# Kernel tuning notes

Measured on AMD Instinct MI355X. Metric: run time of the kernel, lower is better.

## Reference

```python
import jax, jax.numpy as jnp
import numpy as np

NUM_CLASSES = 19  # number of distinct labels in targets (fill_max)


def setup_inputs() -> dict:
    key = jax.random.key(0)
    k1, k2 = jax.random.split(key)
    n, d = 262144, 128
    inputs = jax.random.normal(k1, (n, d), dtype=jnp.float32)
    targets = jax.random.randint(k2, (n,), 0, NUM_CLASSES, dtype=jnp.int64)
    return {"inputs": inputs, "targets": targets}


def reference(inputs, targets):
    # Same math as the O(n^2) torch loop: for each sample i, the center is the
    # mean of all samples sharing targets[i]. Computed as one segment-reduction
    # over labels followed by a gather.
    n = inputs.shape[0]
    sums = jax.ops.segment_sum(inputs, targets, num_segments=NUM_CLASSES)          # [C, d]
    counts = jax.ops.segment_sum(jnp.ones((n,), inputs.dtype), targets,
                                 num_segments=NUM_CLASSES)                          # [C]
    class_centers = sums / counts[:, None]                                          # [C, d]
    centers = class_centers[targets]                                                # [n, d]
    dist_pc = jnp.sqrt(jnp.sum((inputs - centers) ** 2, axis=1))                    # [n]
    return jnp.mean(dist_pc)
```

## Files before the change

### kernel.cpp

```cpp
#include <hip/hip_runtime.h>
#include <math.h>

#define NCLS 19
#define DIM  128
#define CD   (NCLS * DIM)
#define WPB  16

__global__ __launch_bounds__(1024) void k_accum(const float2* __restrict__ in2,
                                                const int* __restrict__ tgt,
                                                float* __restrict__ gsums,
                                                int* __restrict__ gcounts,
                                                int n) {
    __shared__ float ls[WPB * CD];
    __shared__ int   lcnt[WPB * NCLS];
    const int tid  = threadIdx.x;
    const int w    = tid >> 6;
    const int lane = tid & 63;
    float* tbl = &ls[w * CD];
    int*   cnt = &lcnt[w * NCLS];

    for (int i = tid; i < WPB * CD; i += 1024) ls[i] = 0.0f;
    for (int i = tid; i < WPB * NCLS; i += 1024) lcnt[i] = 0;
    __syncthreads();

    const int stride = gridDim.x * WPB;
    for (int row = blockIdx.x * WPB + w; row < n; row += stride) {
        float2 v = in2[(size_t)row * 64 + lane];
        int c = tgt[row];
        float2 cur = *(float2*)&tbl[c * DIM + lane * 2];
        cur.x += v.x;
        cur.y += v.y;
        *(float2*)&tbl[c * DIM + lane * 2] = cur;
        if (lane == 0) cnt[c]++;
    }
    __syncthreads();

    for (int i = tid; i < CD; i += 1024) {
        float s = 0.0f;
        #pragma unroll
        for (int ww = 0; ww < WPB; ww++) s += ls[ww * CD + i];
        unsafeAtomicAdd(&gsums[i], s);
    }
    if (tid < NCLS) {
        int s = 0;
        #pragma unroll
        for (int ww = 0; ww < WPB; ww++) s += lcnt[ww * NCLS + tid];
        atomicAdd(&gcounts[tid], s);
    }
}

__global__ __launch_bounds__(256) void k_dist(const float4* __restrict__ in4,
                                              const int* __restrict__ tgt,
                                              const float* __restrict__ gsums,
                                              const int* __restrict__ gcounts,
                                              float* __restrict__ out,
                                              int n, float inv_n) {
    __shared__ __align__(16) float lcent[CD];
    __shared__ float red[256];
    const int tid = threadIdx.x;

    for (int i = tid; i < CD; i += 256)
        lcent[i] = gsums[i] / (float)gcounts[i >> 7];
    __syncthreads();

    const int l32 = tid & 31;
    const int rib = tid >> 5;
    const int stride = gridDim.x * 8;
    float acc = 0.0f;

    for (int row = blockIdx.x * 8 + rib; row < n; row += stride) {
        float4 v = in4[(size_t)row * 32 + l32];
        int c = tgt[row];
        float4 ce = *(const float4*)&lcent[c * DIM + l32 * 4];
        float dx = v.x - ce.x, dy = v.y - ce.y, dz = v.z - ce.z, dw = v.w - ce.w;
        float d2 = dx * dx + dy * dy + dz * dz + dw * dw;
        for (int off = 16; off > 0; off >>= 1)
            d2 += __shfl_down(d2, off, 32);
        if (l32 == 0) acc += sqrtf(d2);
    }

    red[tid] = acc;
    __syncthreads();
    for (int s = 128; s > 0; s >>= 1) {
        if (tid < s) red[tid] += red[tid + s];
        __syncthreads();
    }
    if (tid == 0) unsafeAtomicAdd(out, red[0] * inv_n);
}

extern "C" void kernel_launch(void* const* d_in, const int* in_sizes, int n_in,
                              void* d_out, int out_size, void* d_ws, size_t ws_size,
                              hipStream_t stream) {
    const float* in  = (const float*)d_in[0];
    const int*   tgt = (const int*)d_in[1];
    const int n = in_sizes[0] / DIM;

    float* gsums   = (float*)d_ws;
    int*   gcounts = (int*)(gsums + CD);
    float* out     = (float*)d_out;

    hipMemsetAsync(d_ws, 0, CD * sizeof(float) + NCLS * sizeof(int), stream);
    hipMemsetAsync(d_out, 0, sizeof(float), stream);

    k_accum<<<256, 1024, 0, stream>>>((const float2*)in, tgt, gsums, gcounts, n);
    k_dist<<<1024, 256, 0, stream>>>((const float4*)in, tgt, gsums, gcounts, out,
                                     n, 1.0f / (float)n);
}
```

Before: 238.5 us.

## Restructure accumulation to 32-lane float4 groups and unroll both kernels by four rows

The accumulation kernel moves from 1024-thread blocks with 64-lane float2 private tables to 256-thread blocks with 32-lane float4 groups, each keeping its own shared-memory table, and the grid doubles to 512 blocks. Both the accumulation and distance loops are unrolled four ways so four row loads are in flight before they are used, aiming to hide global memory latency in this bandwidth-bound pass. Smaller per-block LDS use may allow more blocks per CU, but there are fewer private tables per block and more global atomics from the extra blocks.

```diff
diff --git a/kernel.cpp b/kernel.cpp
--- a/kernel.cpp
+++ b/kernel.cpp
@@ -4,47 +4,70 @@
 #define NCLS 19
 #define DIM  128
 #define CD   (NCLS * DIM)
-#define WPB  16
+#define GPB  8
 
-__global__ __launch_bounds__(1024) void k_accum(const float2* __restrict__ in2,
-                                                const int* __restrict__ tgt,
-                                                float* __restrict__ gsums,
-                                                int* __restrict__ gcounts,
-                                                int n) {
-    __shared__ float ls[WPB * CD];
-    __shared__ int   lcnt[WPB * NCLS];
-    const int tid  = threadIdx.x;
-    const int w    = tid >> 6;
-    const int lane = tid & 63;
-    float* tbl = &ls[w * CD];
-    int*   cnt = &lcnt[w * NCLS];
+__global__ __launch_bounds__(256) void k_accum(const float4* __restrict__ in4,
+                                               const int* __restrict__ tgt,
+                                               float* __restrict__ gsums,
+                                               int* __restrict__ gcounts,
+                                               int n) {
+    __shared__ __align__(16) float ls[GPB * CD];
+    __shared__ int lcnt[GPB * NCLS];
+    const int tid = threadIdx.x;
+    const int g   = tid >> 5;
+    const int l32 = tid & 31;
+    float* tbl = &ls[g * CD];
+    int*   cnt = &lcnt[g * NCLS];
 
-    for (int i = tid; i < WPB * CD; i += 1024) ls[i] = 0.0f;
-    for (int i = tid; i < WPB * NCLS; i += 1024) lcnt[i] = 0;
+    for (int i = tid; i < GPB * CD; i += 256) ls[i] = 0.0f;
+    for (int i = tid; i < GPB * NCLS; i += 256) lcnt[i] = 0;
     __syncthreads();
 
-    const int stride = gridDim.x * WPB;
-    for (int row = blockIdx.x * WPB + w; row < n; row += stride) {
-        float2 v = in2[(size_t)row * 64 + lane];
+    const int stride = gridDim.x * GPB;
+    int row = blockIdx.x * GPB + g;
+
+    for (; row + 3 * stride < n; row += 4 * stride) {
+        float4 v0 = in4[(size_t)(row             ) * 32 + l32];
+        float4 v1 = in4[(size_t)(row +     stride) * 32 + l32];
+        float4 v2 = in4[(size_t)(row + 2 * stride) * 32 + l32];
+        float4 v3 = in4[(size_t)(row + 3 * stride) * 32 + l32];
+        int c0 = tgt[row];
+        int c1 = tgt[row + stride];
+        int c2 = tgt[row + 2 * stride];
+        int c3 = tgt[row + 3 * stride];
+        float4* p;
+        float4 a;
+        p = (float4*)&tbl[c0 * DIM + l32 * 4];
+        a = *p; a.x += v0.x; a.y += v0.y; a.z += v0.z; a.w += v0.w; *p = a;
+        p = (float4*)&tbl[c1 * DIM + l32 * 4];
+        a = *p; a.x += v1.x; a.y += v1.y; a.z += v1.z; a.w += v1.w; *p = a;
+        p = (float4*)&tbl[c2 * DIM + l32 * 4];
+        a = *p; a.x += v2.x; a.y += v2.y; a.z += v2.z; a.w += v2.w; *p = a;
+        p = (float4*)&tbl[c3 * DIM + l32 * 4];
+        a = *p; a.x += v3.x; a.y += v3.y; a.z += v3.z; a.w += v3.w; *p = a;
+        if (l32 == 0) { cnt[c0]++; cnt[c1]++; cnt[c2]++; cnt[c3]++; }
+    }
+    for (; row < n; row += stride) {
+        float4 v = in4[(size_t)row * 32 + l32];
         int c = tgt[row];
-        float2 cur = *(float2*)&tbl[c * DIM + lane * 2];
-        cur.x += v.x;
-        cur.y += v.y;
-        *(float2*)&tbl[c * DIM + lane * 2] = cur;
-        if (lane == 0) cnt[c]++;
+        float4* p = (float4*)&tbl[c * DIM + l32 * 4];
+        float4 a = *p;
+        a.x += v.x; a.y += v.y; a.z += v.z; a.w += v.w;
+        *p = a;
+        if (l32 == 0) cnt[c]++;
     }
     __syncthreads();
 
-    for (int i = tid; i < CD; i += 1024) {
+    for (int i = tid; i < CD; i += 256) {
         float s = 0.0f;
         #pragma unroll
-        for (int ww = 0; ww < WPB; ww++) s += ls[ww * CD + i];
+        for (int gg = 0; gg < GPB; gg++) s += ls[gg * CD + i];
         unsafeAtomicAdd(&gsums[i], s);
     }
     if (tid < NCLS) {
         int s = 0;
         #pragma unroll
-        for (int ww = 0; ww < WPB; ww++) s += lcnt[ww * NCLS + tid];
+        for (int gg = 0; gg < GPB; gg++) s += lcnt[gg * NCLS + tid];
         atomicAdd(&gcounts[tid], s);
     }
 }
@@ -64,11 +87,42 @@
     __syncthreads();
 
     const int l32 = tid & 31;
-    const int rib = tid >> 5;
+    const int g   = tid >> 5;
     const int stride = gridDim.x * 8;
     float acc = 0.0f;
+    int row = blockIdx.x * 8 + g;
 
-    for (int row = blockIdx.x * 8 + rib; row < n; row += stride) {
+    for (; row + 3 * stride < n; row += 4 * stride) {
+        float4 v0 = in4[(size_t)(row             ) * 32 + l32];
+        float4 v1 = in4[(size_t)(row +     stride) * 32 + l32];
+        float4 v2 = in4[(size_t)(row + 2 * stride) * 32 + l32];
+        float4 v3 = in4[(size_t)(row + 3 * stride) * 32 + l32];
+        int c0 = tgt[row];
+        int c1 = tgt[row + stride];
+        int c2 = tgt[row + 2 * stride];
+        int c3 = tgt[row + 3 * stride];
+        float4 e0 = *(const float4*)&lcent[c0 * DIM + l32 * 4];
+        float4 e1 = *(const float4*)&lcent[c1 * DIM + l32 * 4];
+        float4 e2 = *(const float4*)&lcent[c2 * DIM + l32 * 4];
+        float4 e3 = *(const float4*)&lcent[c3 * DIM + l32 * 4];
+        float dx, dy, dz, dw;
+        dx = v0.x - e0.x; dy = v0.y - e0.y; dz = v0.z - e0.z; dw = v0.w - e0.w;
+        float d0 = dx * dx + dy * dy + dz * dz + dw * dw;
+        dx = v1.x - e1.x; dy = v1.y - e1.y; dz = v1.z - e1.z; dw = v1.w - e1.w;
+        float d1 = dx * dx + dy * dy + dz * dz + dw * dw;
+        dx = v2.x - e2.x; dy = v2.y - e2.y; dz = v2.z - e2.z; dw = v2.w - e2.w;
+        float d2 = dx * dx + dy * dy + dz * dz + dw * dw;
+        dx = v3.x - e3.x; dy = v3.y - e3.y; dz = v3.z - e3.z; dw = v3.w - e3.w;
+        float d3 = dx * dx + dy * dy + dz * dz + dw * dw;
+        for (int off = 16; off > 0; off >>= 1) {
+            d0 += __shfl_down(d0, off, 32);
+            d1 += __shfl_down(d1, off, 32);
+            d2 += __shfl_down(d2, off, 32);
+            d3 += __shfl_down(d3, off, 32);
+        }
+        if (l32 == 0) acc += sqrtf(d0) + sqrtf(d1) + sqrtf(d2) + sqrtf(d3);
+    }
+    for (; row < n; row += stride) {
         float4 v = in4[(size_t)row * 32 + l32];
         int c = tgt[row];
         float4 ce = *(const float4*)&lcent[c * DIM + l32 * 4];
@@ -102,7 +156,7 @@
     hipMemsetAsync(d_ws, 0, CD * sizeof(float) + NCLS * sizeof(int), stream);
     hipMemsetAsync(d_out, 0, sizeof(float), stream);
 
-    k_accum<<<256, 1024, 0, stream>>>((const float2*)in, tgt, gsums, gcounts, n);
+    k_accum<<<512, 256, 0, stream>>>((const float4*)in, tgt, gsums, gcounts, n);
     k_dist<<<1024, 256, 0, stream>>>((const float4*)in, tgt, gsums, gcounts, out,
                                      n, 1.0f / (float)n);
 }
```

Result: no change. 234.1 us (-1.8%).

## Accumulate class sums in registers and unroll row loops by two

Applied to the files above, without the earlier changes.

The accumulation kernel drops its per-wave shared-memory tables and keeps all 19 class sums in registers, selected through a wave-uniform label read with readfirstlane. Results are merged into one shared table per block with atomics, then into global memory. The shared-memory footprint shrinks and a read-modify-write to LDS on every row is removed, allowing more blocks per CU. Both kernels now process two rows per iteration for more memory-level parallelism, and grid and block sizes are retuned. The cost is extra register pressure from 38 accumulators plus a chain of compare-select operations per row.

```diff
diff --git a/kernel.cpp b/kernel.cpp
--- a/kernel.cpp
+++ b/kernel.cpp
@@ -4,57 +4,68 @@
 #define NCLS 19
 #define DIM  128
 #define CD   (NCLS * DIM)
-#define WPB  16
 
-__global__ __launch_bounds__(1024) void k_accum(const float2* __restrict__ in2,
-                                                const int* __restrict__ tgt,
-                                                float* __restrict__ gsums,
-                                                int* __restrict__ gcounts,
-                                                int n) {
-    __shared__ float ls[WPB * CD];
-    __shared__ int   lcnt[WPB * NCLS];
+__global__ __launch_bounds__(512, 6) void k_accum(const float2* __restrict__ in2,
+                                                  const int* __restrict__ tgt,
+                                                  float* __restrict__ gsums,
+                                                  int* __restrict__ gcounts,
+                                                  int n) {
+    __shared__ float lsum[CD];
+    __shared__ int   lcnt[NCLS];
     const int tid  = threadIdx.x;
     const int w    = tid >> 6;
     const int lane = tid & 63;
-    float* tbl = &ls[w * CD];
-    int*   cnt = &lcnt[w * NCLS];
 
-    for (int i = tid; i < WPB * CD; i += 1024) ls[i] = 0.0f;
-    for (int i = tid; i < WPB * NCLS; i += 1024) lcnt[i] = 0;
+    float2 acc[NCLS];
+    int    cnt[NCLS];
+    #pragma unroll
+    for (int k = 0; k < NCLS; k++) { acc[k] = make_float2(0.f, 0.f); cnt[k] = 0; }
+
+    for (int i = tid; i < CD; i += 512) lsum[i] = 0.0f;
+    if (tid < NCLS) lcnt[tid] = 0;
     __syncthreads();
 
-    const int stride = gridDim.x * WPB;
-    for (int row = blockIdx.x * WPB + w; row < n; row += stride) {
+    const int wid    = blockIdx.x * 8 + w;
+    const int stride = gridDim.x * 8;
+    int row = wid;
+
+    for (; row + stride < n; row += 2 * stride) {
+        float2 v0 = in2[(size_t)row * 64 + lane];
+        float2 v1 = in2[(size_t)(row + stride) * 64 + lane];
+        int c0 = __builtin_amdgcn_readfirstlane(tgt[row]);
+        int c1 = __builtin_amdgcn_readfirstlane(tgt[row + stride]);
+        #pragma unroll
+        for (int k = 0; k < NCLS; k++) {
+            if (c0 == k) { acc[k].x += v0.x; acc[k].y += v0.y; cnt[k]++; }
+            if (c1 == k) { acc[k].x += v1.x; acc[k].y += v1.y; cnt[k]++; }
+        }
+    }
+    for (; row < n; row += stride) {
         float2 v = in2[(size_t)row * 64 + lane];
-        int c = tgt[row];
-        float2 cur = *(float2*)&tbl[c * DIM + lane * 2];
-        cur.x += v.x;
-        cur.y += v.y;
-        *(float2*)&tbl[c * DIM + lane * 2] = cur;
-        if (lane == 0) cnt[c]++;
+        int c = __builtin_amdgcn_readfirstlane(tgt[row]);
+        #pragma unroll
+        for (int k = 0; k < NCLS; k++)
+            if (c == k) { acc[k].x += v.x; acc[k].y += v.y; cnt[k]++; }
+    }
+
+    #pragma unroll
+    for (int k = 0; k < NCLS; k++) {
+        unsafeAtomicAdd(&lsum[k * DIM + lane * 2    ], acc[k].x);
+        unsafeAtomicAdd(&lsum[k * DIM + lane * 2 + 1], acc[k].y);
+        if (lane == 0 && cnt[k]) atomicAdd(&lcnt[k], cnt[k]);
     }
     __syncthreads();
 
-    for (int i = tid; i < CD; i += 1024) {
-        float s = 0.0f;
-        #pragma unroll
-        for (int ww = 0; ww < WPB; ww++) s += ls[ww * CD + i];
-        unsafeAtomicAdd(&gsums[i], s);
-    }
-    if (tid < NCLS) {
-        int s = 0;
-        #pragma unroll
-        for (int ww = 0; ww < WPB; ww++) s += lcnt[ww * NCLS + tid];
-        atomicAdd(&gcounts[tid], s);
-    }
+    for (int i = tid; i < CD; i += 512) unsafeAtomicAdd(&gsums[i], lsum[i]);
+    if (tid < NCLS) atomicAdd(&gcounts[tid], lcnt[tid]);
 }
 
-__global__ __launch_bounds__(256) void k_dist(const float4* __restrict__ in4,
-                                              const int* __restrict__ tgt,
-                                              const float* __restrict__ gsums,
-                                              const int* __restrict__ gcounts,
-                                              float* __restrict__ out,
-                                              int n, float inv_n) {
+__global__ __launch_bounds__(256, 8) void k_dist(const float4* __restrict__ in4,
+                                                 const int* __restrict__ tgt,
+                                                 const float* __restrict__ gsums,
+                                                 const int* __restrict__ gcounts,
+                                                 float* __restrict__ out,
+                                                 int n, float inv_n) {
     __shared__ __align__(16) float lcent[CD];
     __shared__ float red[256];
     const int tid = threadIdx.x;
@@ -64,11 +75,30 @@
     __syncthreads();
 
     const int l32 = tid & 31;
-    const int rib = tid >> 5;
+    const int g   = tid >> 5;
     const int stride = gridDim.x * 8;
     float acc = 0.0f;
+    int row = blockIdx.x * 8 + g;
 
-    for (int row = blockIdx.x * 8 + rib; row < n; row += stride) {
+    for (; row + stride < n; row += 2 * stride) {
+        float4 va = in4[(size_t)row * 32 + l32];
+        float4 vb = in4[(size_t)(row + stride) * 32 + l32];
+        int ca = tgt[row];
+        int cb = tgt[row + stride];
+        float4 ea = *(const float4*)&lcent[ca * DIM + l32 * 4];
+        float4 eb = *(const float4*)&lcent[cb * DIM + l32 * 4];
+        float dx, dy, dz, dw;
+        dx = va.x - ea.x; dy = va.y - ea.y; dz = va.z - ea.z; dw = va.w - ea.w;
+        float d0 = dx * dx + dy * dy + dz * dz + dw * dw;
+        dx = vb.x - eb.x; dy = vb.y - eb.y; dz = vb.z - eb.z; dw = vb.w - eb.w;
+        float d1 = dx * dx + dy * dy + dz * dz + dw * dw;
+        for (int off = 16; off > 0; off >>= 1) {
+            d0 += __shfl_down(d0, off, 32);
+            d1 += __shfl_down(d1, off, 32);
+        }
+        if (l32 == 0) acc += sqrtf(d0) + sqrtf(d1);
+    }
+    for (; row < n; row += stride) {
         float4 v = in4[(size_t)row * 32 + l32];
         int c = tgt[row];
         float4 ce = *(const float4*)&lcent[c * DIM + l32 * 4];
@@ -102,7 +132,7 @@
     hipMemsetAsync(d_ws, 0, CD * sizeof(float) + NCLS * sizeof(int), stream);
     hipMemsetAsync(d_out, 0, sizeof(float), stream);
 
-    k_accum<<<256, 1024, 0, stream>>>((const float2*)in, tgt, gsums, gcounts, n);
-    k_dist<<<1024, 256, 0, stream>>>((const float4*)in, tgt, gsums, gcounts, out,
+    k_accum<<<1024, 512, 0, stream>>>((const float2*)in, tgt, gsums, gcounts, n);
+    k_dist<<<2048, 256, 0, stream>>>((const float4*)in, tgt, gsums, gcounts, out,
                                      n, 1.0f / (float)n);
 }
```

Result: slower. 355.2 us (+48.9%).
